# Optimization experiments

Hardware: AMD Instinct MI355X
Metric: run time of the kernel (lower is better)

## Reference

```python
import jax, jax.numpy as jnp
import numpy as np

N, C = 65536, 1000

def setup_inputs() -> dict:
    key = jax.random.key(0)
    k1, k2 = jax.random.split(key)
    x = jax.random.normal(k1, (N, C), dtype=jnp.float32)
    P_matrix = jax.random.uniform(k2, (N, C), dtype=jnp.float32)
    return {"x": x, "P_matrix": P_matrix}

def reference(x, P_matrix):
    # Original: loss = sum_k mean_i( P[i,k] * CE(x_i, target=k) )
    #         = -(1/N) * sum_{i,k} P[i,k] * log_softmax(x)[i,k]
    n = x.shape[0]
    logp = jax.nn.log_softmax(x, axis=-1)  # single pass instead of per-class loop
    loss = -jnp.sum(P_matrix * logp) / n
    return loss
```

## Files before the change

### kernel.cpp

```cpp
#include <hip/hip_runtime.h>
#include <hip/hip_bf16.h>
#include <math.h>


#define NROWS  65536
#define NC     1000
#define NC4    250
#define NBLK   (NROWS / 4)
#define LOG2E  1.4426950408889634f
#define LN2    0.6931471805599453f

typedef float f32x4 __attribute__((ext_vector_type(4)));

__global__ __launch_bounds__(256) void ebem_row_kernel(
    const float* __restrict__ x, const float* __restrict__ p,
    float* __restrict__ blk_out)
{
    const int lane = threadIdx.x & 63;
    const int wave = threadIdx.x >> 6;
    const long long row = (long long)blockIdx.x * 4 + wave;

    const f32x4* xr = (const f32x4*)(x + row * (long long)NC);
    const f32x4* pr = (const f32x4*)(p + row * (long long)NC);

    f32x4 xs[4], ps[4];
    float m = -INFINITY;

    #pragma unroll
    for (int k = 0; k < 4; ++k) {
        const int idx = lane + 64 * k;
        if (idx < NC4) xs[k] = __builtin_nontemporal_load(&xr[idx]);
    }
    #pragma unroll
    for (int k = 0; k < 4; ++k) {
        const int idx = lane + 64 * k;
        if (idx < NC4) ps[k] = __builtin_nontemporal_load(&pr[idx]);
    }

    #pragma unroll
    for (int k = 0; k < 4; ++k) {
        const int idx = lane + 64 * k;
        if (idx < NC4)
            m = fmaxf(m, fmaxf(fmaxf(xs[k].x, xs[k].y),
                               fmaxf(xs[k].z, xs[k].w)));
    }

    #pragma unroll
    for (int off = 32; off; off >>= 1)
        m = fmaxf(m, __shfl_xor(m, off));

    float s = 0.f, dot = 0.f, psum = 0.f;
    #pragma unroll
    for (int k = 0; k < 4; ++k) {
        const int idx = lane + 64 * k;
        if (idx < NC4) {
            s += exp2f((xs[k].x - m) * LOG2E);
            s += exp2f((xs[k].y - m) * LOG2E);
            s += exp2f((xs[k].z - m) * LOG2E);
            s += exp2f((xs[k].w - m) * LOG2E);
            dot  += ps[k].x * xs[k].x + ps[k].y * xs[k].y
                  + ps[k].z * xs[k].z + ps[k].w * xs[k].w;
            psum += ps[k].x + ps[k].y + ps[k].z + ps[k].w;
        }
    }

    #pragma unroll
    for (int off = 32; off; off >>= 1) {
        s    += __shfl_xor(s, off);
        dot  += __shfl_xor(dot, off);
        psum += __shfl_xor(psum, off);
    }

    __shared__ float part[4];
    if (lane == 0) {
        const float lse = m + log2f(s) * LN2;
        part[wave] = psum * lse - dot;
    }
    __syncthreads();
    if (threadIdx.x == 0)
        blk_out[blockIdx.x] = (part[0] + part[1]) + (part[2] + part[3]);
}

__global__ __launch_bounds__(1024) void ebem_reduce_kernel(
    const float* __restrict__ blk_vals, float* __restrict__ out)
{
    const int tid  = threadIdx.x;
    const int lane = tid & 63;
    const int wid  = tid >> 6;

    double acc = 0.0;
    #pragma unroll
    for (int i = tid; i < NBLK; i += 1024)
        acc += (double)blk_vals[i];

    #pragma unroll
    for (int off = 32; off; off >>= 1)
        acc += __shfl_xor(acc, off);

    __shared__ double sm[16];
    if (lane == 0) sm[wid] = acc;
    __syncthreads();

    if (tid < 16) {
        acc = sm[tid];
        #pragma unroll
        for (int off = 8; off; off >>= 1)
            acc += __shfl_xor(acc, off);
        if (tid == 0)
            out[0] = (float)(acc / (double)NROWS);
    }
}

extern "C" void kernel_launch(void* const* d_in, const int* in_sizes, int n_in,
                              void* d_out, int out_size, void* d_ws, size_t ws_size,
                              hipStream_t stream) {
    const float* x = (const float*)d_in[0];
    const float* p = (const float*)d_in[1];
    float* blk_vals = (float*)d_ws;
    float* out = (float*)d_out;

    ebem_row_kernel<<<NBLK, 256, 0, stream>>>(x, p, blk_vals);
    ebem_reduce_kernel<<<1, 1024, 0, stream>>>(blk_vals, out);
}
```

Baseline: 88.41 us.

## Process eight rows per wave with double-buffered register prefetch

Each wave now handles eight rows instead of one. It prefetches the next row's x and P into a second register buffer while computing the current row's loss, then accumulates the per-row losses before the block reduction. This cuts the grid size by a factor of eight and is meant to hide load latency inside each wave. In exchange it roughly doubles register use per thread, which can lower occupancy, and the fewer waves in flight may expose more memory latency.

Result: no change. 89.03 us (+0.7%).

```diff
diff --git a/kernel.cpp b/kernel.cpp
--- a/kernel.cpp
+++ b/kernel.cpp
@@ -6,26 +6,20 @@
 #define NROWS  65536
 #define NC     1000
 #define NC4    250
-#define NBLK   (NROWS / 4)
+#define RPW    8
+#define NWAVES (NROWS / RPW)
+#define NBLK   (NWAVES / 4)
 #define LOG2E  1.4426950408889634f
 #define LN2    0.6931471805599453f
 
 typedef float f32x4 __attribute__((ext_vector_type(4)));
 
-__global__ __launch_bounds__(256) void ebem_row_kernel(
+__device__ __forceinline__ void load_row(
     const float* __restrict__ x, const float* __restrict__ p,
-    float* __restrict__ blk_out)
+    long long row, int lane, f32x4 (&xs)[4], f32x4 (&ps)[4])
 {
-    const int lane = threadIdx.x & 63;
-    const int wave = threadIdx.x >> 6;
-    const long long row = (long long)blockIdx.x * 4 + wave;
-
     const f32x4* xr = (const f32x4*)(x + row * (long long)NC);
     const f32x4* pr = (const f32x4*)(p + row * (long long)NC);
-
-    f32x4 xs[4], ps[4];
-    float m = -INFINITY;
-
     #pragma unroll
     for (int k = 0; k < 4; ++k) {
         const int idx = lane + 64 * k;
@@ -36,7 +30,12 @@
         const int idx = lane + 64 * k;
         if (idx < NC4) ps[k] = __builtin_nontemporal_load(&pr[idx]);
     }
+}
 
+__device__ __forceinline__ float row_loss(
+    const f32x4 (&xs)[4], const f32x4 (&ps)[4], int lane)
+{
+    float m = -INFINITY;
     #pragma unroll
     for (int k = 0; k < 4; ++k) {
         const int idx = lane + 64 * k;
@@ -44,7 +43,6 @@
             m = fmaxf(m, fmaxf(fmaxf(xs[k].x, xs[k].y),
                                fmaxf(xs[k].z, xs[k].w)));
     }
-
     #pragma unroll
     for (int off = 32; off; off >>= 1)
         m = fmaxf(m, __shfl_xor(m, off));
@@ -63,19 +61,41 @@
             psum += ps[k].x + ps[k].y + ps[k].z + ps[k].w;
         }
     }
-
     #pragma unroll
     for (int off = 32; off; off >>= 1) {
         s    += __shfl_xor(s, off);
         dot  += __shfl_xor(dot, off);
         psum += __shfl_xor(psum, off);
     }
+    const float lse = m + log2f(s) * LN2;
+    return psum * lse - dot;
+}
+
+__global__ __launch_bounds__(256) void ebem_row_kernel(
+    const float* __restrict__ x, const float* __restrict__ p,
+    float* __restrict__ blk_out)
+{
+    const int lane = threadIdx.x & 63;
+    const int wave = threadIdx.x >> 6;
+    const long long row0 = ((long long)blockIdx.x * 4 + wave) * RPW;
+
+    f32x4 xa[4], pa[4], xb[4], pb[4];
+    float acc = 0.f;
+
+    load_row(x, p, row0, lane, xa, pa);
+    #pragma unroll
+    for (int r = 0; r < RPW; ++r) {
+        if ((r & 1) == 0) {
+            if (r + 1 < RPW) load_row(x, p, row0 + r + 1, lane, xb, pb);
+            acc += row_loss(xa, pa, lane);
+        } else {
+            if (r + 1 < RPW) load_row(x, p, row0 + r + 1, lane, xa, pa);
+            acc += row_loss(xb, pb, lane);
+        }
+    }
 
     __shared__ float part[4];
-    if (lane == 0) {
-        const float lse = m + log2f(s) * LN2;
-        part[wave] = psum * lse - dot;
-    }
+    if (lane == 0) part[wave] = acc;
     __syncthreads();
     if (threadIdx.x == 0)
         blk_out[blockIdx.x] = (part[0] + part[1]) + (part[2] + part[3]);
```
